# Kernel optimization log

Hardware: AMD Instinct MI355X
Metric: run time of the kernel (lower is better)

The kernel has to match this reference:

```python
import jax, jax.numpy as jnp
import numpy as np

def setup_inputs() -> dict:
    key = jax.random.key(0)
    k1, k2, k3, k4 = jax.random.split(key, 4)
    B, S, E, H = 4, 4096, 1024, 64
    x = jax.random.normal(k1, (B, S, E), dtype=jnp.float32)
    scale = E ** -0.5  # keep activations well-scaled like trained Linear weights
    Wq = jax.random.normal(k2, (E, H), dtype=jnp.float32) * scale
    Wk = jax.random.normal(k3, (E, H), dtype=jnp.float32) * scale
    Wv = jax.random.normal(k4, (E, H), dtype=jnp.float32) * scale
    return {"x": x, "Wq": Wq, "Wk": Wk, "Wv": Wv}

def reference(x, Wq, Wk, Wv):
    # x: [B, S, E]; W*: [E, H]
    B, S, E = x.shape
    H = Wq.shape[1]
    q = jnp.einsum('bse,eh->bsh', x, Wq)
    k = jnp.einsum('bse,eh->bsh', x, Wk)
    v = jnp.einsum('bse,eh->bsh', x, Wv)
    att = jnp.einsum('bqh,bkh->bqk', q, k) * (H ** -0.5)  # [B, S, S]
    causal = jnp.tril(jnp.ones((S, S), dtype=bool))
    att = jnp.where(causal, att, -jnp.inf)
    att = jax.nn.softmax(att, axis=-1)
    # dropout p=0.0 (eval-mode): identity
    return jnp.einsum('bqk,bkh->bqh', att, v)
```

## Files before the change

### kernel.cpp

```cpp
#include <hip/hip_runtime.h>


using short8 = __attribute__((ext_vector_type(8))) short;
using f32x4  = __attribute__((ext_vector_type(4))) float;

#define MFMA16(A, B, C) __builtin_amdgcn_mfma_f32_16x16x32_bf16((A), (B), (C), 0, 0, 0)

typedef const __attribute__((address_space(1))) void* gas_ptr;
typedef __attribute__((address_space(3))) void*       las_ptr;

__device__ __forceinline__ void gload16(const void* g, void* l) {
    __builtin_amdgcn_global_load_lds((gas_ptr)g, (las_ptr)l, 16, 0, 0);
}

__device__ __forceinline__ unsigned short f2bf(float f) {
    unsigned u = __builtin_bit_cast(unsigned, f);
    u += 0x7fffu + ((u >> 16) & 1u);
    return (unsigned short)(u >> 16);
}
__device__ __forceinline__ float bf2f(unsigned short u) {
    unsigned v = ((unsigned)u) << 16;
    return __builtin_bit_cast(float, v);
}

__global__ __launch_bounds__(256) void transpose_w(
    const float* __restrict__ Wq,
    const float* __restrict__ Wk,
    const float* __restrict__ Wv,
    unsigned short* __restrict__ Ws,
    unsigned short* __restrict__ Vt)
{
    int o = blockIdx.x * 256 + threadIdx.x;
    if (o < 196608) {
        int j    = o & 7;
        int l    = (o >> 3) & 63;
        int g    = (o >> 9) & 7;
        int rem  = o >> 12;
        int mt   = rem % 3;
        int sk   = rem / 3;
        int c    = g >> 2, nt = g & 3;
        int quad = l >> 4, n  = l & 15;
        int e    = sk * 64 + c * 32 + quad * 8 + j;
        int h    = nt * 16 + n;
        const float* W = (mt == 0) ? Wq : (mt == 1) ? Wk : Wv;
        Ws[o] = f2bf(W[e * 64 + h]);
    } else {
        int jj  = o - 196608;
        int b   = jj >> 16;
        int rem = jj & 65535;
        int h   = 64 + (rem >> 12);
        int s   = rem & 4095;
        Vt[((size_t)(b * 80 + h)) * 4096 + s] = (h == 64) ? 0x3F80 : 0;
    }
}

__global__ __launch_bounds__(128, 2) void proj_all(
    const float* __restrict__ x,
    const unsigned short* __restrict__ Ws,
    unsigned short* __restrict__ Qo,
    unsigned short* __restrict__ Ko,
    unsigned short* __restrict__ Vto)
{
    const int m0   = blockIdx.x * 32;
    const int tid  = threadIdx.x;
    const int lane = tid & 63;
    const int wv   = tid >> 6;
    const int quad = lane >> 4;
    const int n    = lane & 15;

    __shared__ __align__(16) float xs[2][8][64][4];
    __shared__ __align__(16) short wf[2][24][64][8];

    const f32x4 zero4 = {0.f, 0.f, 0.f, 0.f};
    f32x4 acc[3][4];
    #pragma unroll
    for (int mt = 0; mt < 3; ++mt)
        #pragma unroll
        for (int nt = 0; nt < 4; ++nt) acc[mt][nt] = zero4;

    auto stage = [&](int k0, int p) {
        #pragma unroll
        for (int it = 0; it < 4; ++it) {
            int i     = wv + 2 * it;
            int Rl    = 4 * i + (lane >> 4);
            int chunk = (lane & 15) ^ ((Rl & 3) << 2);
            gload16(x + (size_t)(m0 + Rl) * 1024 + k0 + chunk * 4, &xs[p][i][0][0]);
        }
        int sk = k0 >> 6;
        #pragma unroll
        for (int it = 0; it < 12; ++it) {
            int f = wv + 2 * it;
            gload16(Ws + (((size_t)sk * 24 + f) << 9) + lane * 8, &wf[p][f][0][0]);
        }
    };

    int p = 0;
    stage(0, 0);
    __syncthreads();

    for (int k0 = 0; k0 < 1024; k0 += 64) {
        if (k0 < 960) stage(k0 + 64, p ^ 1);

        int sub = n & 3, s = sub << 2;
        const float* xp = &xs[p][wv * 4 + (n >> 2)][0][0] + sub * 64;
        f32x4 u0 = *(const f32x4*)(xp + (((2 * quad)     ^ s) << 2));
        f32x4 u1 = *(const f32x4*)(xp + (((2 * quad + 1) ^ s) << 2));
        f32x4 u2 = *(const f32x4*)(xp + (((8 + 2 * quad) ^ s) << 2));
        f32x4 u3 = *(const f32x4*)(xp + (((9 + 2 * quad) ^ s) << 2));
        short8 a0, a1;
        #pragma unroll
        for (int j = 0; j < 4; ++j) {
            a0[j]     = (short)f2bf(u0[j]);
            a0[4 + j] = (short)f2bf(u1[j]);
            a1[j]     = (short)f2bf(u2[j]);
            a1[4 + j] = (short)f2bf(u3[j]);
        }

        #pragma unroll
        for (int mt = 0; mt < 3; ++mt)
            #pragma unroll
            for (int nt = 0; nt < 4; ++nt) {
                acc[mt][nt] = MFMA16(a0, *(const short8*)(&wf[p][mt * 8 + nt][lane][0]),     acc[mt][nt]);
                acc[mt][nt] = MFMA16(a1, *(const short8*)(&wf[p][mt * 8 + 4 + nt][lane][0]), acc[mt][nt]);
            }

        __syncthreads();
        p ^= 1;
    }

    #pragma unroll
    for (int nt = 0; nt < 4; ++nt) {
        #pragma unroll
        for (int r = 0; r < 4; ++r) {
            int m = m0 + wv * 16 + quad * 4 + r;
            int h = nt * 16 + n;
            Qo[(size_t)m * 64 + h] = f2bf(acc[0][nt][r]);
            Ko[(size_t)m * 64 + h] = f2bf(acc[1][nt][r]);
            int b = m >> 12, s2 = m & 4095;
            Vto[((size_t)(b * 80 + h)) * 4096 + s2] = f2bf(acc[2][nt][r]);
        }
    }
}

template <int SPLIT>
__device__ __forceinline__ void attn_body(
    const unsigned short* __restrict__ Q,
    const unsigned short* __restrict__ K,
    const unsigned short* __restrict__ Vt,
    float* __restrict__ dst,
    int b, int r0, int kt0, int kt1)
{
    const int tid  = threadIdx.x;
    const int lane = tid & 63;
    const int wv   = tid >> 6;
    const int quad = lane >> 4;
    const int n    = lane & 15;
    const int ktmask = r0 >> 6;

    __shared__ __align__(16) short kf[2][8][64][8];
    __shared__ __align__(16) short vf[2][10][64][8];
    __shared__ __align__(16) unsigned short pbuf[4][32][72];

    short8 qa[2][2];
    #pragma unroll
    for (int rg = 0; rg < 2; ++rg) {
        const unsigned short* qp =
            Q + (size_t)(b * 4096 + r0 + wv * 32 + rg * 16 + n) * 64 + quad * 8;
        #pragma unroll
        for (int j = 0; j < 8; ++j) {
            qa[rg][0][j] = (short)f2bf(bf2f(qp[j])      * 0.125f);
            qa[rg][1][j] = (short)f2bf(bf2f(qp[32 + j]) * 0.125f);
        }
    }

    const f32x4 zero4 = {0.f, 0.f, 0.f, 0.f};
    f32x4 oacc[2][5];
    #pragma unroll
    for (int rg = 0; rg < 2; ++rg)
        #pragma unroll
        for (int nt = 0; nt < 5; ++nt) oacc[rg][nt] = zero4;

    const unsigned short* kbase = K  + ((size_t)b * 4096 + n) * 64 + quad * 8;
    const unsigned short* vbase = Vt + ((size_t)b * 80 + n) * 4096 + quad * 8;

    auto stage = [&](int kt, int p) {
        #pragma unroll
        for (int it = 0; it < 5; ++it) {
            int f = wv + 4 * it;
            if (f < 8) {
                int c = f >> 2, nt = f & 3;
                gload16(kbase + (size_t)(kt * 64 + nt * 16) * 64 + c * 32, &kf[p][f][0][0]);
            } else if (f < 18) {
                int pnl = f - 8;
                int nt = pnl >> 1, c = pnl & 1;
                gload16(vbase + (size_t)nt * 16 * 4096 + kt * 64 + c * 32, &vf[p][pnl][0][0]);
            }
        }
    };

    int p = 0;
    stage(kt0, 0);
    __syncthreads();

    for (int kt = kt0; kt <= kt1; ++kt) {
        if (kt < kt1) stage(kt + 1, p ^ 1);

        short8 kfr[8];
        #pragma unroll
        for (int f = 0; f < 8; ++f)
            kfr[f] = *(const short8*)(&kf[p][f][lane][0]);

        #pragma unroll
        for (int rg = 0; rg < 2; ++rg) {
            f32x4 sacc[4] = {zero4, zero4, zero4, zero4};
            #pragma unroll
            for (int nt = 0; nt < 4; ++nt) {
                sacc[nt] = MFMA16(qa[rg][0], kfr[nt],     sacc[nt]);
                sacc[nt] = MFMA16(qa[rg][1], kfr[4 + nt], sacc[nt]);
            }
            if (kt >= ktmask) {
                int qg = r0 + wv * 32 + rg * 16 + quad * 4;
                #pragma unroll
                for (int nt = 0; nt < 4; ++nt)
                    #pragma unroll
                    for (int r = 0; r < 4; ++r) {
                        int key = kt * 64 + nt * 16 + n;
                        if (key > qg + r) sacc[nt][r] = -1e30f;
                    }
            }
            #pragma unroll
            for (int nt = 0; nt < 4; ++nt)
                #pragma unroll
                for (int r = 0; r < 4; ++r)
                    pbuf[wv][rg * 16 + quad * 4 + r][nt * 16 + n] = f2bf(__expf(sacc[nt][r]));
        }

        short8 vfr[10];
        #pragma unroll
        for (int pnl = 0; pnl < 10; ++pnl)
            vfr[pnl] = *(const short8*)(&vf[p][pnl][lane][0]);

        #pragma unroll
        for (int rg = 0; rg < 2; ++rg) {
            short8 pa0 = *(const short8*)(&pbuf[wv][rg * 16 + n][quad * 8]);
            short8 pa1 = *(const short8*)(&pbuf[wv][rg * 16 + n][32 + quad * 8]);
            #pragma unroll
            for (int nt = 0; nt < 5; ++nt) {
                oacc[rg][nt] = MFMA16(pa0, vfr[2 * nt],     oacc[rg][nt]);
                oacc[rg][nt] = MFMA16(pa1, vfr[2 * nt + 1], oacc[rg][nt]);
            }
        }

        __syncthreads();
        p ^= 1;
    }

    if (SPLIT) {
        #pragma unroll
        for (int rg = 0; rg < 2; ++rg)
            #pragma unroll
            for (int r = 0; r < 4; ++r) {
                int row = wv * 32 + rg * 16 + quad * 4 + r;
                #pragma unroll
                for (int nt = 0; nt < 4; ++nt)
                    dst[row * 64 + nt * 16 + n] = oacc[rg][nt][r];
                if (n == 0) dst[8192 + row] = oacc[rg][4][r];
            }
    } else {
        #pragma unroll
        for (int rg = 0; rg < 2; ++rg)
            #pragma unroll
            for (int r = 0; r < 4; ++r) {
                float l   = __shfl(oacc[rg][4][r], quad * 16, 64);
                float inv = 1.f / l;
                int q = r0 + wv * 32 + rg * 16 + quad * 4 + r;
                #pragma unroll
                for (int nt = 0; nt < 4; ++nt)
                    dst[(size_t)(b * 4096 + q) * 64 + nt * 16 + n] = oacc[rg][nt][r] * inv;
            }
    }
}

__global__ __launch_bounds__(256, 2) void attn_part(
    const unsigned short* __restrict__ Q,
    const unsigned short* __restrict__ K,
    const unsigned short* __restrict__ Vt,
    float* __restrict__ Part)
{
    int id = blockIdx.x;
    int b  = id & 3;
    int t  = 143 - (id >> 2);
    int g  = 0;
    while (2 * (g + 1) * (g + 2) <= t) ++g;
    int u  = t - 2 * g * (g + 1);
    int qt = 4 * g + u / (g + 1);
    int c  = u - (u / (g + 1)) * (g + 1);

    int r0  = qt * 128;
    int kt0 = c * 8;
    int kt1 = min(kt0 + 7, 2 * qt + 1);

    float* dst = Part + (size_t)(b * 144 + t) * 8320;
    attn_body<1>(Q, K, Vt, dst, b, r0, kt0, kt1);
}

__global__ __launch_bounds__(256, 2) void attn_mono(
    const unsigned short* __restrict__ Q,
    const unsigned short* __restrict__ K,
    const unsigned short* __restrict__ Vt,
    float* __restrict__ out)
{
    int id = blockIdx.x;
    int qt = 31 - (id >> 2);
    int b  = id & 3;
    attn_body<0>(Q, K, Vt, out, b, qt * 128, 0, 2 * qt + 1);
}

__global__ __launch_bounds__(256) void combine(
    const float* __restrict__ Part, float* __restrict__ out)
{
    int id    = blockIdx.x;
    int slice = id & 3;
    int bq    = id >> 2;
    int b     = bq & 3;
    int qt    = bq >> 2;
    int g     = qt >> 2;
    int nc    = g + 1;
    int t0    = 2 * g * (g + 1) + (qt & 3) * (g + 1);
    const float* P0 = Part + (size_t)(b * 144 + t0) * 8320;

    int tid = threadIdx.x;

    __shared__ float invden[32];
    if (tid < 32) {
        float d[8] = {0, 0, 0, 0, 0, 0, 0, 0};
        #pragma unroll 8
        for (int c = 0; c < 8; ++c)
            if (c < nc) d[c] = P0[c * 8320 + 8192 + slice * 32 + tid];
        invden[tid] = 1.f / (((d[0] + d[1]) + (d[2] + d[3])) +
                             ((d[4] + d[5]) + (d[6] + d[7])));
    }

    float acc[8] = {0, 0, 0, 0, 0, 0, 0, 0};
    const float* Pe = P0 + slice * 2048 + tid;
    for (int c = 0; c < nc; ++c) {
        const float* Pc = Pe + (size_t)c * 8320;
        #pragma unroll
        for (int j = 0; j < 8; ++j)
            acc[j] += Pc[j * 256];
    }

    __syncthreads();
    #pragma unroll
    for (int j = 0; j < 8; ++j) {
        int e   = slice * 2048 + j * 256 + tid;
        int row = (e >> 6) & 31;
        out[((size_t)b * 4096 + qt * 128 + slice * 32) * 64 + (size_t)(j * 256 + tid)]
            = acc[j] * invden[row];
    }
}

extern "C" void kernel_launch(void* const* d_in, const int* in_sizes, int n_in,
                              void* d_out, int out_size, void* d_ws, size_t ws_size,
                              hipStream_t stream) {
    const float* x  = (const float*)d_in[0];
    const float* Wq = (const float*)d_in[1];
    const float* Wk = (const float*)d_in[2];
    const float* Wv = (const float*)d_in[3];
    float* outp = (float*)d_out;
    unsigned short* ws = (unsigned short*)d_ws;

    unsigned short* Qw  = ws;
    unsigned short* Kw  = ws + 1048576;
    unsigned short* Vtw = ws + 2097152;
    unsigned short* Wsp = ws + 3407872;

    size_t part_off = ((size_t)3604480 * 2 + 255) & ~(size_t)255;
    size_t need     = part_off + (size_t)4 * 144 * 8320 * 4;
    float* Part = (float*)((char*)d_ws + part_off);

    transpose_w<<<dim3(1792), dim3(256), 0, stream>>>(Wq, Wk, Wv, Wsp, Vtw);
    proj_all<<<dim3(512), dim3(128), 0, stream>>>(x, Wsp, Qw, Kw, Vtw);

    if (ws_size >= need) {
        attn_part<<<dim3(576), dim3(256), 0, stream>>>(Qw, Kw, Vtw, Part);
        combine<<<dim3(512), dim3(256), 0, stream>>>(Part, outp);
    } else {
        attn_mono<<<dim3(128), dim3(256), 0, stream>>>(Qw, Kw, Vtw, outp);
    }
}
```

Baseline: 155.0 us.

## Compute softmax row sums in registers instead of a ones-column MFMA

The softmax denominator is no longer produced by an extra all-ones V column fed through MFMA. It is now accumulated from the bf16-rounded probabilities in registers and reduced across lanes with shuffles at the end. This removes one fifth of the PV MFMAs, the fifth V panel load, and the setup writes that filled the padding rows. The Q scale folds in log2(e) so the hardware exp2 can replace __expf, the MFMA loops are reordered to load K/V fragments per tile, and launch bounds request three blocks per CU, which trades register headroom for occupancy.

```diff
diff --git a/kernel.cpp b/kernel.cpp
--- a/kernel.cpp
+++ b/kernel.cpp
@@ -23,12 +23,21 @@
     return __builtin_bit_cast(float, v);
 }
 
+__device__ __forceinline__ float exp2_fast(float x) {
+#if __has_builtin(__builtin_amdgcn_exp2f)
+    return __builtin_amdgcn_exp2f(x);
+#else
+    float r;
+    asm("v_exp_f32 %0, %1" : "=v"(r) : "v"(x));
+    return r;
+#endif
+}
+
 __global__ __launch_bounds__(256) void transpose_w(
     const float* __restrict__ Wq,
     const float* __restrict__ Wk,
     const float* __restrict__ Wv,
-    unsigned short* __restrict__ Ws,
-    unsigned short* __restrict__ Vt)
+    unsigned short* __restrict__ Ws)
 {
     int o = blockIdx.x * 256 + threadIdx.x;
     if (o < 196608) {
@@ -44,13 +53,6 @@
         int h    = nt * 16 + n;
         const float* W = (mt == 0) ? Wq : (mt == 1) ? Wk : Wv;
         Ws[o] = f2bf(W[e * 64 + h]);
-    } else {
-        int jj  = o - 196608;
-        int b   = jj >> 16;
-        int rem = jj & 65535;
-        int h   = 64 + (rem >> 12);
-        int s   = rem & 4095;
-        Vt[((size_t)(b * 80 + h)) * 4096 + s] = (h == 64) ? 0x3F80 : 0;
     }
 }
 
@@ -158,7 +160,7 @@
     const int ktmask = r0 >> 6;
 
     __shared__ __align__(16) short kf[2][8][64][8];
-    __shared__ __align__(16) short vf[2][10][64][8];
+    __shared__ __align__(16) short vf[2][8][64][8];
     __shared__ __align__(16) unsigned short pbuf[4][32][72];
 
     short8 qa[2][2];
@@ -168,29 +170,30 @@
             Q + (size_t)(b * 4096 + r0 + wv * 32 + rg * 16 + n) * 64 + quad * 8;
         #pragma unroll
         for (int j = 0; j < 8; ++j) {
-            qa[rg][0][j] = (short)f2bf(bf2f(qp[j])      * 0.125f);
-            qa[rg][1][j] = (short)f2bf(bf2f(qp[32 + j]) * 0.125f);
+            qa[rg][0][j] = (short)f2bf(bf2f(qp[j])      * 0.18033688f);
+            qa[rg][1][j] = (short)f2bf(bf2f(qp[32 + j]) * 0.18033688f);
         }
     }
 
     const f32x4 zero4 = {0.f, 0.f, 0.f, 0.f};
-    f32x4 oacc[2][5];
+    f32x4 oacc[2][4];
+    float lacc[2][4];
     #pragma unroll
     for (int rg = 0; rg < 2; ++rg)
         #pragma unroll
-        for (int nt = 0; nt < 5; ++nt) oacc[rg][nt] = zero4;
+        for (int nt = 0; nt < 4; ++nt) { oacc[rg][nt] = zero4; lacc[rg][nt] = 0.f; }
 
     const unsigned short* kbase = K  + ((size_t)b * 4096 + n) * 64 + quad * 8;
     const unsigned short* vbase = Vt + ((size_t)b * 80 + n) * 4096 + quad * 8;
 
     auto stage = [&](int kt, int p) {
         #pragma unroll
-        for (int it = 0; it < 5; ++it) {
+        for (int it = 0; it < 4; ++it) {
             int f = wv + 4 * it;
             if (f < 8) {
                 int c = f >> 2, nt = f & 3;
                 gload16(kbase + (size_t)(kt * 64 + nt * 16) * 64 + c * 32, &kf[p][f][0][0]);
-            } else if (f < 18) {
+            } else {
                 int pnl = f - 8;
                 int nt = pnl >> 1, c = pnl & 1;
                 gload16(vbase + (size_t)nt * 16 * 4096 + kt * 64 + c * 32, &vf[p][pnl][0][0]);
@@ -205,55 +208,83 @@
     for (int kt = kt0; kt <= kt1; ++kt) {
         if (kt < kt1) stage(kt + 1, p ^ 1);
 
-        short8 kfr[8];
-        #pragma unroll
-        for (int f = 0; f < 8; ++f)
-            kfr[f] = *(const short8*)(&kf[p][f][lane][0]);
-
-        #pragma unroll
-        for (int rg = 0; rg < 2; ++rg) {
-            f32x4 sacc[4] = {zero4, zero4, zero4, zero4};
-            #pragma unroll
-            for (int nt = 0; nt < 4; ++nt) {
-                sacc[nt] = MFMA16(qa[rg][0], kfr[nt],     sacc[nt]);
-                sacc[nt] = MFMA16(qa[rg][1], kfr[4 + nt], sacc[nt]);
-            }
-            if (kt >= ktmask) {
+        f32x4 sacc[2][4];
+        #pragma unroll
+        for (int rg = 0; rg < 2; ++rg)
+            #pragma unroll
+            for (int nt = 0; nt < 4; ++nt) sacc[rg][nt] = zero4;
+
+        #pragma unroll
+        for (int nt = 0; nt < 4; ++nt) {
+            short8 ka = *(const short8*)(&kf[p][nt][lane][0]);
+            short8 kb = *(const short8*)(&kf[p][4 + nt][lane][0]);
+            #pragma unroll
+            for (int rg = 0; rg < 2; ++rg) {
+                sacc[rg][nt] = MFMA16(qa[rg][0], ka, sacc[rg][nt]);
+                sacc[rg][nt] = MFMA16(qa[rg][1], kb, sacc[rg][nt]);
+            }
+        }
+
+        if (kt >= ktmask) {
+            #pragma unroll
+            for (int rg = 0; rg < 2; ++rg) {
                 int qg = r0 + wv * 32 + rg * 16 + quad * 4;
                 #pragma unroll
                 for (int nt = 0; nt < 4; ++nt)
                     #pragma unroll
                     for (int r = 0; r < 4; ++r) {
                         int key = kt * 64 + nt * 16 + n;
-                        if (key > qg + r) sacc[nt][r] = -1e30f;
+                        if (key > qg + r) sacc[rg][nt][r] = -1e30f;
                     }
             }
-            #pragma unroll
-            for (int nt = 0; nt < 4; ++nt)
+        }
+
+        #pragma unroll
+        for (int rg = 0; rg < 2; ++rg)
+            #pragma unroll
+            for (int r = 0; r < 4; ++r) {
+                float rs = 0.f;
                 #pragma unroll
-                for (int r = 0; r < 4; ++r)
-                    pbuf[wv][rg * 16 + quad * 4 + r][nt * 16 + n] = f2bf(__expf(sacc[nt][r]));
-        }
-
-        short8 vfr[10];
-        #pragma unroll
-        for (int pnl = 0; pnl < 10; ++pnl)
-            vfr[pnl] = *(const short8*)(&vf[p][pnl][lane][0]);
-
+                for (int nt = 0; nt < 4; ++nt) {
+                    unsigned short pv = f2bf(exp2_fast(sacc[rg][nt][r]));
+                    pbuf[wv][rg * 16 + quad * 4 + r][nt * 16 + n] = pv;
+                    rs += bf2f(pv);
+                }
+                lacc[rg][r] += rs;
+            }
+
+        short8 pa[2][2];
         #pragma unroll
         for (int rg = 0; rg < 2; ++rg) {
-            short8 pa0 = *(const short8*)(&pbuf[wv][rg * 16 + n][quad * 8]);
-            short8 pa1 = *(const short8*)(&pbuf[wv][rg * 16 + n][32 + quad * 8]);
-            #pragma unroll
-            for (int nt = 0; nt < 5; ++nt) {
-                oacc[rg][nt] = MFMA16(pa0, vfr[2 * nt],     oacc[rg][nt]);
-                oacc[rg][nt] = MFMA16(pa1, vfr[2 * nt + 1], oacc[rg][nt]);
+            pa[rg][0] = *(const short8*)(&pbuf[wv][rg * 16 + n][quad * 8]);
+            pa[rg][1] = *(const short8*)(&pbuf[wv][rg * 16 + n][32 + quad * 8]);
+        }
+        #pragma unroll
+        for (int nt = 0; nt < 4; ++nt) {
+            short8 va = *(const short8*)(&vf[p][2 * nt][lane][0]);
+            short8 vb = *(const short8*)(&vf[p][2 * nt + 1][lane][0]);
+            #pragma unroll
+            for (int rg = 0; rg < 2; ++rg) {
+                oacc[rg][nt] = MFMA16(pa[rg][0], va, oacc[rg][nt]);
+                oacc[rg][nt] = MFMA16(pa[rg][1], vb, oacc[rg][nt]);
             }
         }
 
         __syncthreads();
         p ^= 1;
     }
+
+    #pragma unroll
+    for (int rg = 0; rg < 2; ++rg)
+        #pragma unroll
+        for (int r = 0; r < 4; ++r) {
+            float v = lacc[rg][r];
+            v += __shfl_xor(v, 1);
+            v += __shfl_xor(v, 2);
+            v += __shfl_xor(v, 4);
+            v += __shfl_xor(v, 8);
+            lacc[rg][r] = v;
+        }
 
     if (SPLIT) {
         #pragma unroll
@@ -264,15 +295,14 @@
                 #pragma unroll
                 for (int nt = 0; nt < 4; ++nt)
                     dst[row * 64 + nt * 16 + n] = oacc[rg][nt][r];
-                if (n == 0) dst[8192 + row] = oacc[rg][4][r];
+                if (n == 0) dst[8192 + row] = lacc[rg][r];
             }
     } else {
         #pragma unroll
         for (int rg = 0; rg < 2; ++rg)
             #pragma unroll
             for (int r = 0; r < 4; ++r) {
-                float l   = __shfl(oacc[rg][4][r], quad * 16, 64);
-                float inv = 1.f / l;
+                float inv = 1.f / lacc[rg][r];
                 int q = r0 + wv * 32 + rg * 16 + quad * 4 + r;
                 #pragma unroll
                 for (int nt = 0; nt < 4; ++nt)
@@ -281,7 +311,7 @@
     }
 }
 
-__global__ __launch_bounds__(256, 2) void attn_part(
+__global__ __launch_bounds__(256, 3) void attn_part(
     const unsigned short* __restrict__ Q,
     const unsigned short* __restrict__ K,
     const unsigned short* __restrict__ Vt,
@@ -304,7 +334,7 @@
     attn_body<1>(Q, K, Vt, dst, b, r0, kt0, kt1);
 }
 
-__global__ __launch_bounds__(256, 2) void attn_mono(
+__global__ __launch_bounds__(256, 3) void attn_mono(
     const unsigned short* __restrict__ Q,
     const unsigned short* __restrict__ K,
     const unsigned short* __restrict__ Vt,
@@ -379,7 +409,7 @@
     size_t need     = part_off + (size_t)4 * 144 * 8320 * 4;
     float* Part = (float*)((char*)d_ws + part_off);
 
-    transpose_w<<<dim3(1792), dim3(256), 0, stream>>>(Wq, Wk, Wv, Wsp, Vtw);
+    transpose_w<<<dim3(768), dim3(256), 0, stream>>>(Wq, Wk, Wv, Wsp);
     proj_all<<<dim3(512), dim3(128), 0, stream>>>(x, Wsp, Qw, Kw, Vtw);
 
     if (ws_size >= need) {
```

After: 149.4 us. 1.04x faster.
